# Optimization experiments

Measured on AMD Instinct MI355X. Metric: run time of the kernel, lower is better.

## Reference

```python
import jax, jax.numpy as jnp
import numpy as np


def _grid_neighbors(H, W):
    # 4-neighbor grid adjacency for the Mesh([H, W]) graph
    idx = np.arange(H * W).reshape(H, W)
    p = np.full((H + 2, W + 2), -1, dtype=np.int64)
    p[1:-1, 1:-1] = idx
    nbrs = np.stack([p[0:H, 1:W + 1], p[2:H + 2, 1:W + 1], p[1:H + 1, 0:W], p[1:H + 1, 2:W + 2]], axis=-1).reshape(H * W, 4)
    mask = (nbrs >= 0).astype(np.float32)
    return np.where(nbrs >= 0, nbrs, 0), mask, mask.sum(-1) + 1.0


def _conv(x, w, b):
    y = jax.lax.conv_general_dilated(x, w, (1, 1), 'SAME', dimension_numbers=('NCHW', 'OIHW', 'NCHW'))
    return y + b[None, :, None, None]


def _dconv(x, w1, b1, w2, b2):
    return jax.nn.relu(_conv(jax.nn.relu(_conv(x, w1, b1)), w2, b2))


def _maxpool(x):
    return jax.lax.reduce_window(x, -jnp.inf, jax.lax.max, (1, 1, 2, 2), (1, 1, 2, 2), 'VALID')


def _convT(x, w, b):
    # kernel=2, stride=2 transposed conv (non-overlapping upsample)
    y = jax.lax.conv_transpose(x, w, (2, 2), 'VALID', dimension_numbers=('NCHW', 'HWIO', 'NCHW'))
    return y + b[None, :, None, None]


def _gconv(X, W, b, nbrs, mask, deg):
    # mesh graph conv: D^-1 (A + I) X W, irregular gather over grid adjacency
    g = X[:, nbrs, :]                                          # [B, N, 4, C]
    agg = ((g * mask[None, :, :, None]).sum(2) + X) / deg[None, :, None]
    return jax.nn.relu(jnp.einsum('bnc,cd->bnd', agg, W) + b[None, None, :])


def _forward(x, d1w1, d1b1, d1w2, d1b2, d2w1, d2b1, d2w2, d2b2, md1w, md1b, md2w, md2b, mbw, mbb, mu1w, mu1b, mu2w, mu2b, u3tw, u3tb, u3w1, u3b1, u3w2, u3b2, u4tw, u4tb, u4w1, u4b1, u4w2, u4b2, ow, ob):
    b1 = _dconv(x, d1w1, d1b1, d1w2, d1b2)                     # [1,64,256,256]
    b2 = _dconv(_maxpool(b1), d2w1, d2b1, d2w2, d2b2)          # [1,128,128,128]
    fe = _maxpool(b2)                                           # [1,128,64,64]
    fe = jnp.pad(fe, ((0, 0), (0, 0), (1, 1), (1, 1)))          # pad -> 66x66
    B, C, Hm, Wm = fe.shape
    nbrs, mask, deg = _grid_neighbors(Hm, Wm)
    nbrs, mask, deg = jnp.asarray(nbrs), jnp.asarray(mask), jnp.asarray(deg)
    X = fe.reshape(B, C, Hm * Wm).transpose(0, 2, 1)            # [1, 4356, 128]
    bp1 = _gconv(X, md1w, md1b, nbrs, mask, deg)                # 256 (skip)
    bp2 = _gconv(bp1, md2w, md2b, nbrs, mask, deg)              # 512 (skip)
    Xb = _gconv(bp2, mbw, mbb, nbrs, mask, deg)                 # 1024 mesh bottleneck
    X = _gconv(Xb, mu1w, mu1b, nbrs, mask, deg) + bp2           # 512
    X = _gconv(X, mu2w, mu2b, nbrs, mask, deg) + bp1            # 256
    fe = X.transpose(0, 2, 1).reshape(B, 256, Hm, Wm)[:, :, 1:-1, 1:-1]  # unpad -> 64x64
    u3 = _convT(fe, u3tw, u3tb)                                 # [1,128,128,128]
    fe = _dconv(jnp.concatenate([b2, u3], 1), u3w1, u3b1, u3w2, u3b2)
    u4 = _convT(fe, u4tw, u4tb)                                 # [1,64,256,256]
    fe = _dconv(jnp.concatenate([b1, u4], 1), u4w1, u4b1, u4w2, u4b2)
    return _conv(fe, ow, ob)[:, 0]                              # [1,256,256]


def setup_inputs():
    ks = iter(jax.random.split(jax.random.key(0), 40))
    def W(shape, fan_in):
        return jax.random.normal(next(ks), shape, jnp.float32) * np.float32(np.sqrt(2.0 / fan_in))
    def Z(n):
        return jnp.zeros((n,), jnp.float32)
    return {
        'x': jax.random.normal(next(ks), (1, 3, 256, 256), jnp.float32),
        'd1w1': W((64, 3, 3, 3), 27), 'd1b1': Z(64), 'd1w2': W((64, 64, 3, 3), 576), 'd1b2': Z(64),
        'd2w1': W((128, 64, 3, 3), 576), 'd2b1': Z(128), 'd2w2': W((128, 128, 3, 3), 1152), 'd2b2': Z(128),
        'md1w': W((128, 256), 128), 'md1b': Z(256),
        'md2w': W((256, 512), 256), 'md2b': Z(512),
        'mbw': W((512, 1024), 512), 'mbb': Z(1024),
        'mu1w': W((1024, 512), 1024), 'mu1b': Z(512),
        'mu2w': W((512, 256), 512), 'mu2b': Z(256),
        'u3tw': W((2, 2, 256, 128), 1024), 'u3tb': Z(128),
        'u3w1': W((128, 256, 3, 3), 2304), 'u3b1': Z(128), 'u3w2': W((128, 128, 3, 3), 1152), 'u3b2': Z(128),
        'u4tw': W((2, 2, 128, 64), 512), 'u4tb': Z(64),
        'u4w1': W((64, 128, 3, 3), 1152), 'u4b1': Z(64), 'u4w2': W((64, 64, 3, 3), 576), 'u4b2': Z(64),
        'ow': W((1, 64, 3, 3), 576), 'ob': Z(1),
    }


def reference(x, d1w1, d1b1, d1w2, d1b2, d2w1, d2b1, d2w2, d2b2, md1w, md1b, md2w, md2b, mbw, mbb, mu1w, mu1b, mu2w, mu2b, u3tw, u3tb, u3w1, u3b1, u3w2, u3b2, u4tw, u4tb, u4w1, u4b1, u4w2, u4b2, ow, ob):
    return _forward(x, d1w1, d1b1, d1w2, d1b2, d2w1, d2b1, d2w2, d2b2, md1w, md1b, md2w, md2b, mbw, mbb, mu1w, mu1b, mu2w, mu2b, u3tw, u3tb, u3w1, u3b1, u3w2, u3b2, u4tw, u4tb, u4w1, u4b1, u4w2, u4b2, ow, ob)
```

## Files before the change

### kernel.cpp

```cpp
#include <hip/hip_runtime.h>
#include <cstddef>

#define TPB 256

typedef __attribute__((ext_vector_type(8))) short short8;
typedef __attribute__((ext_vector_type(4))) float f32x4;

__device__ inline unsigned short f2bf(float f) {
    unsigned int u = __builtin_bit_cast(unsigned int, f);
    u += 0x7fffu + ((u >> 16) & 1u);
    return (unsigned short)(u >> 16);
}
__device__ inline float bf2f(unsigned short h) {
    unsigned int u = ((unsigned int)h) << 16;
    return __builtin_bit_cast(float, u);
}

struct TapOffs { int o[9]; };

template<int CHUNKS>
__global__ __launch_bounds__(TPB) void k_conv3f(
    const unsigned short* __restrict__ A0, const unsigned short* __restrict__ Wf,
    const float* __restrict__ bias, unsigned short* __restrict__ O0,
    int AP, int tilesX, int OMS, int OP, int NTtot)
{
    constexpr int Cs  = CHUNKS * 64;
    constexpr int KC2 = CHUNKS * 2;
    __shared__ unsigned short Bs[2][CHUNKS * 4096];

    int lane = threadIdx.x & 63, wave = threadIdx.x >> 6;
    int ml = lane & 15, kq = lane >> 4;
    int nb = blockIdx.y;
    int tileX = blockIdx.x % tilesX, gy = blockIdx.x / tilesX;
    int gx0 = tileX * 64 + wave * 16;

    const unsigned short* Abase = A0 + (size_t)(gy - 1) * AP
                                     + (size_t)(gx0 + ml - 1) * Cs + kq * 8;

    f32x4 acc[4];
    #pragma unroll
    for (int nt = 0; nt < 4; ++nt) acc[nt] = (f32x4){0.f, 0.f, 0.f, 0.f};

    auto stageB = [&](int tap, int buf) {
        unsigned short* bd = Bs[buf];
        #pragma unroll
        for (int it = 0; it < CHUNKS * 2; ++it) {
            int u = threadIdx.x + it * TPB;
            int e = u * 8;
            int ch = e >> 12;
            int rem = e & 4095;
            int q = rem >> 11;
            int rem2 = rem & 2047;
            int ntg = rem2 >> 9;
            int r = rem2 & 511;
            const unsigned short* src = Wf
                + ((size_t)(tap * KC2 + ch * 2 + q) * NTtot + nb * 4 + ntg) * 512 + r;
            *(int4*)&bd[e] = *(const int4*)src;
        }
    };

    stageB(0, 0);
    __syncthreads();
    #pragma unroll
    for (int tap = 0; tap < 9; ++tap) {
        if (tap < 8) stageB(tap + 1, (tap + 1) & 1);
        int ky = tap / 3, kx = tap - (tap / 3) * 3;
        const unsigned short* Ar = Abase + (size_t)ky * AP + kx * Cs;
        const unsigned short* Bb = &Bs[tap & 1][lane * 8];
        #pragma unroll
        for (int ch = 0; ch < CHUNKS; ++ch) {
            #pragma unroll
            for (int q = 0; q < 2; ++q) {
                short8 b[4];
                #pragma unroll
                for (int nt = 0; nt < 4; ++nt)
                    b[nt] = *(const short8*)(Bb + ch * 4096 + q * 2048 + nt * 512);
                short8 a = *(const short8*)(Ar + ch * 64 + q * 32);
                #pragma unroll
                for (int nt = 0; nt < 4; ++nt)
                    acc[nt] = __builtin_amdgcn_mfma_f32_16x16x32_bf16(a, b[nt], acc[nt], 0, 0, 0);
            }
        }
        __syncthreads();
    }

    unsigned short* Orow = O0 + (size_t)gy * OP + (size_t)nb * 64;
    int gx = gx0 + kq * 4;
    #pragma unroll
    for (int nt = 0; nt < 4; ++nt) {
        float bv = bias[nb * 64 + nt * 16 + ml];
        #pragma unroll
        for (int r = 0; r < 4; ++r) {
            float v = fmaxf(acc[nt][r] + bv, 0.f);
            Orow[(size_t)(gx + r) * OMS + nt * 16 + ml] = f2bf(v);
        }
    }
}

template<int KCW>
__global__ __launch_bounds__(TPB) void k_gemmS(
    const unsigned short* __restrict__ A0, const unsigned short* __restrict__ Wf,
    const float* __restrict__ bias, const unsigned short* __restrict__ resid,
    unsigned short* __restrict__ O0, int NTtot,
    int AP, int Wimg, int OMS, int OP, int relu, int ct, int ctDy, int ctDx)
{
    constexpr int K = KCW * 128;
    __shared__ float red[12 * 4 * 64 * 4];
    int lane = threadIdx.x & 63, wave = threadIdx.x >> 6;
    int ml = lane & 15, kq = lane >> 4;
    int m0 = blockIdx.x * 64, nb = blockIdx.y;

    const unsigned short* Wb = Wf;
    unsigned short* Ob = O0;
    if (ct) {
        int tp = blockIdx.z;
        Wb += (size_t)(tp * KCW * 4) * NTtot * 512;
        int dy = 1 - (tp >> 1), dx = 1 - (tp & 1);
        Ob += (size_t)dy * ctDy + (size_t)dx * ctDx;
    }

    const unsigned short* Ap[4];
    #pragma unroll
    for (int i = 0; i < 4; ++i) {
        int mf = (wave + i) & 3;
        int m = m0 + mf * 16;
        int y = m / Wimg, x = m - y * Wimg;
        Ap[i] = A0 + (size_t)y * AP + (size_t)(x + ml) * K + wave * (KCW * 32) + kq * 8;
    }
    const unsigned short* Bp = Wb + ((size_t)(wave * KCW) * NTtot + nb * 4) * 512 + lane * 8;

    f32x4 acc[4][4];
    #pragma unroll
    for (int i = 0; i < 4; ++i)
        #pragma unroll
        for (int nt = 0; nt < 4; ++nt) acc[i][nt] = (f32x4){0.f, 0.f, 0.f, 0.f};

    #pragma unroll
    for (int q = 0; q < KCW; ++q) {
        short8 b[4];
        #pragma unroll
        for (int nt = 0; nt < 4; ++nt)
            b[nt] = *(const short8*)(Bp + ((size_t)q * NTtot + nt) * 512);
        short8 a[4];
        #pragma unroll
        for (int i = 0; i < 4; ++i)
            a[i] = *(const short8*)(Ap[i] + q * 32);
        #pragma unroll
        for (int i = 0; i < 4; ++i)
            #pragma unroll
            for (int nt = 0; nt < 4; ++nt)
                acc[i][nt] = __builtin_amdgcn_mfma_f32_16x16x32_bf16(a[i], b[nt], acc[i][nt], 0, 0, 0);
    }

    #pragma unroll
    for (int i = 1; i < 4; ++i) {
        int s = wave * 3 + (i - 1);
        #pragma unroll
        for (int nt = 0; nt < 4; ++nt)
            *(f32x4*)&red[(((s * 4 + nt) * 64) + lane) * 4] = acc[i][nt];
    }
    __syncthreads();
    #pragma unroll
    for (int w2 = 0; w2 < 4; ++w2) {
        if (w2 == wave) continue;
        int i = (wave - w2) & 3;
        int s = w2 * 3 + (i - 1);
        #pragma unroll
        for (int nt = 0; nt < 4; ++nt) {
            f32x4 v = *(const f32x4*)&red[(((s * 4 + nt) * 64) + lane) * 4];
            acc[0][nt] += v;
        }
    }

    int mrow = m0 + wave * 16 + kq * 4;
    int y = mrow / Wimg, x = mrow - y * Wimg;
    unsigned short* Ot = Ob + (size_t)y * OP + (size_t)x * OMS + nb * 64;
    const unsigned short* Rt = resid ? resid + (size_t)mrow * OMS + nb * 64 : nullptr;
    #pragma unroll
    for (int nt = 0; nt < 4; ++nt) {
        float bv = bias[nb * 64 + nt * 16 + ml];
        #pragma unroll
        for (int r = 0; r < 4; ++r) {
            float v = acc[0][nt][r] + bv;
            if (relu) v = fmaxf(v, 0.f);
            if (Rt) v += bf2f(Rt[(size_t)r * OMS + nt * 16 + ml]);
            Ot[(size_t)r * OMS + nt * 16 + ml] = f2bf(v);
        }
    }
}

template<int KC>
__global__ __launch_bounds__(TPB) void k_gemmN(
    const unsigned short* __restrict__ A0, const unsigned short* __restrict__ Wf,
    const float* __restrict__ bias, unsigned short* __restrict__ O0,
    int Cs, int AP, int Wimg, int OMS, int OP, int NTtot, int relu,
    int ct, int ctDy, int ctDx)
{
    int lane = threadIdx.x & 63, wave = threadIdx.x >> 6;
    int ml = lane & 15, kq = lane >> 4;
    int nb = blockIdx.y;

    const unsigned short* Wb = Wf;
    unsigned short* Ob = O0;
    if (ct) {
        int tp = blockIdx.z;
        Wb += (size_t)(tp * KC) * NTtot * 512;
        int dy = 1 - (tp >> 1), dx = 1 - (tp & 1);
        Ob += (size_t)dy * ctDy + (size_t)dx * ctDx;
    }
    int m0 = blockIdx.x * 64 + wave * 16;
    int y = m0 / Wimg, x = m0 - y * Wimg;
    const unsigned short* Arow = A0 + (size_t)y * AP + (size_t)(x + ml) * Cs + kq * 8;
    const unsigned short* Bp = Wb + (size_t)(nb * 4) * 512 + lane * 8;

    f32x4 acc[4];
    #pragma unroll
    for (int nt = 0; nt < 4; ++nt) acc[nt] = (f32x4){0.f, 0.f, 0.f, 0.f};

    #pragma unroll
    for (int q = 0; q < KC; ++q) {
        short8 b[4];
        #pragma unroll
        for (int nt = 0; nt < 4; ++nt)
            b[nt] = *(const short8*)(Bp + ((size_t)q * NTtot + nt) * 512);
        short8 a = *(const short8*)(Arow + q * 32);
        #pragma unroll
        for (int nt = 0; nt < 4; ++nt)
            acc[nt] = __builtin_amdgcn_mfma_f32_16x16x32_bf16(a, b[nt], acc[nt], 0, 0, 0);
    }

    unsigned short* Ot = Ob + (size_t)y * OP + (size_t)(x + kq * 4) * OMS + (size_t)nb * 64;
    #pragma unroll
    for (int nt = 0; nt < 4; ++nt) {
        float bv = bias[nb * 64 + nt * 16 + ml];
        #pragma unroll
        for (int r = 0; r < 4; ++r) {
            float v = acc[nt][r] + bv;
            if (relu) v = fmaxf(v, 0.f);
            Ot[(size_t)r * OMS + nt * 16 + ml] = f2bf(v);
        }
    }
}

template<int MW, int KC>
__global__ __launch_bounds__(TPB) void k_gemm(
    const unsigned short* __restrict__ A0, const unsigned short* __restrict__ Wf,
    const float* __restrict__ bias, unsigned short* __restrict__ O0,
    int Cs, int AP, int Wimg, int OMS, int OP,
    int T, TapOffs toffs, int NTtot, int relu)
{
    int lane = threadIdx.x & 63, wave = threadIdx.x >> 6;
    int ml = lane & 15, kq = lane >> 4;
    int nb = blockIdx.y;
    const unsigned short* WbB = Wf + (size_t)(nb * 4) * 512 + lane * 8;

    int fy[MW], fx[MW];
    const unsigned short* Af[MW];
    #pragma unroll
    for (int f = 0; f < MW; ++f) {
        int mf = (blockIdx.x * 4 + wave) * (16 * MW) + f * 16;
        int y = mf / Wimg, x = mf - y * Wimg;
        fy[f] = y; fx[f] = x;
        Af[f] = A0 + (size_t)y * AP + (size_t)(x + ml) * Cs + kq * 8;
    }

    f32x4 acc[MW][4];
    #pragma unroll
    for (int f = 0; f < MW; ++f)
        #pragma unroll
        for (int nt = 0; nt < 4; ++nt) acc[f][nt] = (f32x4){0.f, 0.f, 0.f, 0.f};

    for (int tp = 0; tp < T; ++tp) {
        int toff = toffs.o[tp];
        const unsigned short* Wt = WbB + (size_t)(tp * KC) * NTtot * 512;
        #pragma unroll
        for (int q = 0; q < KC; ++q) {
            short8 b[4];
            #pragma unroll
            for (int nt = 0; nt < 4; ++nt)
                b[nt] = *(const short8*)(Wt + (size_t)q * NTtot * 512 + nt * 512);
            short8 a[MW];
            #pragma unroll
            for (int f = 0; f < MW; ++f)
                a[f] = *(const short8*)(Af[f] + toff + q * 32);
            #pragma unroll
            for (int f = 0; f < MW; ++f)
                #pragma unroll
                for (int nt = 0; nt < 4; ++nt)
                    acc[f][nt] = __builtin_amdgcn_mfma_f32_16x16x32_bf16(a[f], b[nt], acc[f][nt], 0, 0, 0);
        }
    }

    #pragma unroll
    for (int f = 0; f < MW; ++f) {
        unsigned short* Ot = O0 + (size_t)fy[f] * OP + (size_t)(fx[f] + kq * 4) * OMS + (size_t)nb * 64;
        #pragma unroll
        for (int nt = 0; nt < 4; ++nt) {
            float bv = bias[nb * 64 + nt * 16 + ml];
            #pragma unroll
            for (int r = 0; r < 4; ++r) {
                float v = acc[f][nt][r] + bv;
                if (relu) v = fmaxf(v, 0.f);
                Ot[(size_t)r * OMS + nt * 16 + ml] = f2bf(v);
            }
        }
    }
}

struct PackArgs {
    const float* w[15];
    int cum[16];
    int mode[15], KC[15], NT[15], K[15], N[15];
};
__global__ __launch_bounds__(TPB) void k_pack_all(
    PackArgs pa, unsigned short* __restrict__ dst, int total)
{
    int idx = blockIdx.x * TPB + threadIdx.x;
    if (idx >= total) return;
    int e = 0;
    #pragma unroll
    for (int i = 1; i < 15; ++i) e += (idx >= pa.cum[i]);
    int local = idx - pa.cum[e];
    const float* w = pa.w[e];
    int KC = pa.KC[e], NT = pa.NT[e], K = pa.K[e], N = pa.N[e], mode = pa.mode[e];

    int j = local & 7, l = (local >> 3) & 63;
    int r = local >> 9;
    int ntg = r % NT; int r2 = r / NT;
    int q = r2 % KC; int tp = r2 / KC;
    int k = q * 32 + (l >> 4) * 8 + j;
    int n = ntg * 16 + (l & 15);
    float v = 0.f;
    if (mode == 0) { int ky = tp / 3, kx = tp % 3; v = w[(size_t)(n * K + k) * 9 + ky * 3 + kx]; }
    else if (mode == 1) { v = w[(size_t)k * N + n]; }
    else if (mode == 2) { v = w[((size_t)tp * K + k) * N + n]; }
    else { if (k < 27) { int tap = k / 3, c = k % 3; int ky = tap / 3, kx = tap % 3;
                         v = w[((n * 3 + c) * 3 + ky) * 3 + kx]; } }
    dst[idx] = f2bf(v);
}

struct ZArgs { int off[10]; int cum[11]; int W2[10]; int H2[10]; int Cs[10]; };
__global__ __launch_bounds__(TPB) void k_zero_all(
    ZArgs za, unsigned short* __restrict__ W, int total)
{
    int idx = blockIdx.x * TPB + threadIdx.x;
    if (idx >= total) return;
    int e = 0;
    #pragma unroll
    for (int i = 1; i < 10; ++i) e += (idx >= za.cum[i]);
    int local = idx - za.cum[e];
    int W2 = za.W2[e], H2 = za.H2[e], Cs = za.Cs[e];
    int topbot = 2 * W2 * Cs;
    int iy, ix, c;
    if (local < topbot) {
        int row = local / (W2 * Cs); int rest = local - row * (W2 * Cs);
        iy = row ? (H2 - 1) : 0; ix = rest / Cs; c = rest - (rest / Cs) * Cs;
    } else {
        int idx2 = local - topbot;
        int per = (H2 - 2) * Cs;
        int side = idx2 / per; int rest = idx2 - side * per;
        iy = 1 + rest / Cs; ix = side ? (W2 - 1) : 0; c = rest - (rest / Cs) * Cs;
    }
    W[(size_t)za.off[e] + ((size_t)iy * W2 + ix) * Cs + c] = 0;
}

__global__ __launch_bounds__(TPB) void k_im2col(
    const float* __restrict__ x, unsigned short* __restrict__ xcol)
{
    int idx = blockIdx.x * TPB + threadIdx.x;
    if (idx >= 65536 * 32) return;
    int k = idx & 31, m = idx >> 5;
    int y = m >> 8, xx = m & 255;
    float v = 0.f;
    if (k < 27) {
        int tap = k / 3, c = k - tap * 3;
        int ty = tap / 3, tx = tap % 3;
        int yy = y + ty - 1, xp = xx + tx - 1;
        if (yy >= 0 && yy < 256 && xp >= 0 && xp < 256)
            v = x[c * 65536 + yy * 256 + xp];
    }
    xcol[idx] = f2bf(v);
}

__global__ __launch_bounds__(TPB) void k_maxpool(
    const unsigned short* __restrict__ inI, unsigned short* __restrict__ outI,
    int Wo, int C4, int CsIn, int inPitch, int CsOut, int outPitch, int total)
{
    int idx = blockIdx.x * TPB + threadIdx.x;
    if (idx >= total) return;
    int c4 = idx % C4; int p = idx / C4;
    int x = p % Wo, y = p / Wo;
    const unsigned short* ip = inI + (size_t)(2 * y) * inPitch + (size_t)(2 * x) * CsIn + c4 * 4;
    ushort4 a = *(const ushort4*)(ip);
    ushort4 b = *(const ushort4*)(ip + CsIn);
    ushort4 c = *(const ushort4*)(ip + inPitch);
    ushort4 d = *(const ushort4*)(ip + inPitch + CsIn);
    ushort4 o;
    o.x = f2bf(fmaxf(fmaxf(bf2f(a.x), bf2f(b.x)), fmaxf(bf2f(c.x), bf2f(d.x))));
    o.y = f2bf(fmaxf(fmaxf(bf2f(a.y), bf2f(b.y)), fmaxf(bf2f(c.y), bf2f(d.y))));
    o.z = f2bf(fmaxf(fmaxf(bf2f(a.z), bf2f(b.z)), fmaxf(bf2f(c.z), bf2f(d.z))));
    o.w = f2bf(fmaxf(fmaxf(bf2f(a.w), bf2f(b.w)), fmaxf(bf2f(c.w), bf2f(d.w))));
    *(ushort4*)(outI + (size_t)y * outPitch + (size_t)x * CsOut + c4 * 4) = o;
}

__global__ __launch_bounds__(TPB) void k_gagg(
    const unsigned short* __restrict__ X, unsigned short* __restrict__ agg,
    int C, int total)
{
    int idx = blockIdx.x * TPB + threadIdx.x;
    if (idx >= total) return;
    int C4 = C >> 2;
    int c4 = idx % C4; int n = idx / C4;
    int i = n / 66, j = n - i * 66;
    size_t base = (size_t)n * C + c4 * 4;
    ushort4 s = *(const ushort4*)(X + base);
    float v0 = bf2f(s.x), v1 = bf2f(s.y), v2 = bf2f(s.z), v3 = bf2f(s.w);
    float cnt = 1.f;
    if (i > 0)  { ushort4 u = *(const ushort4*)(X + base - (size_t)66 * C);
                  v0 += bf2f(u.x); v1 += bf2f(u.y); v2 += bf2f(u.z); v3 += bf2f(u.w); cnt += 1.f; }
    if (i < 65) { ushort4 u = *(const ushort4*)(X + base + (size_t)66 * C);
                  v0 += bf2f(u.x); v1 += bf2f(u.y); v2 += bf2f(u.z); v3 += bf2f(u.w); cnt += 1.f; }
    if (j > 0)  { ushort4 u = *(const ushort4*)(X + base - C);
                  v0 += bf2f(u.x); v1 += bf2f(u.y); v2 += bf2f(u.z); v3 += bf2f(u.w); cnt += 1.f; }
    if (j < 65) { ushort4 u = *(const ushort4*)(X + base + C);
                  v0 += bf2f(u.x); v1 += bf2f(u.y); v2 += bf2f(u.z); v3 += bf2f(u.w); cnt += 1.f; }
    float inv = 1.f / cnt;
    ushort4 o;
    o.x = f2bf(v0 * inv); o.y = f2bf(v1 * inv); o.z = f2bf(v2 * inv); o.w = f2bf(v3 * inv);
    *(ushort4*)(agg + base) = o;
}

__global__ __launch_bounds__(TPB) void k_outconv(
    const unsigned short* __restrict__ vI, const float* __restrict__ ow,
    const float* __restrict__ ob, float* __restrict__ out)
{
    __shared__ float wl[576];
    for (int i = threadIdx.x; i < 576; i += TPB) wl[i] = ow[i];
    __syncthreads();
    int p = blockIdx.x * TPB + threadIdx.x;
    int y = p >> 8, x = p & 255;
    float acc = ob[0];
    #pragma unroll
    for (int ky = 0; ky < 3; ++ky)
        #pragma unroll
        for (int kx = 0; kx < 3; ++kx) {
            const unsigned short* ip = vI + (size_t)((y + ky - 1) * 258 + (x + kx - 1)) * 64;
            int wb = ky * 3 + kx;
            for (int c = 0; c < 64; c += 4) {
                ushort4 uv = *(const ushort4*)(ip + c);
                acc += bf2f(uv.x) * wl[c * 9 + wb] + bf2f(uv.y) * wl[(c + 1) * 9 + wb]
                     + bf2f(uv.z) * wl[(c + 2) * 9 + wb] + bf2f(uv.w) * wl[(c + 3) * 9 + wb];
            }
        }
    out[p] = acc;
}

static inline TapOffs zero_toffs() { TapOffs t = {}; return t; }

extern "C" void kernel_launch(void* const* d_in, const int* in_sizes, int n_in,
                              void* d_out, int out_size, void* d_ws, size_t ws_size,
                              hipStream_t stream) {
    const float* x    = (const float*)d_in[0];
    const float* d1w1 = (const float*)d_in[1];  const float* d1b1 = (const float*)d_in[2];
    const float* d1w2 = (const float*)d_in[3];  const float* d1b2 = (const float*)d_in[4];
    const float* d2w1 = (const float*)d_in[5];  const float* d2b1 = (const float*)d_in[6];
    const float* d2w2 = (const float*)d_in[7];  const float* d2b2 = (const float*)d_in[8];
    const float* md1w = (const float*)d_in[9];  const float* md1b = (const float*)d_in[10];
    const float* md2w = (const float*)d_in[11]; const float* md2b = (const float*)d_in[12];
    const float* mbw  = (const float*)d_in[13]; const float* mbb  = (const float*)d_in[14];
    const float* mu1w = (const float*)d_in[15]; const float* mu1b = (const float*)d_in[16];
    const float* mu2w = (const float*)d_in[17]; const float* mu2b = (const float*)d_in[18];
    const float* u3tw = (const float*)d_in[19]; const float* u3tb = (const float*)d_in[20];
    const float* u3w1 = (const float*)d_in[21]; const float* u3b1 = (const float*)d_in[22];
    const float* u3w2 = (const float*)d_in[23]; const float* u3b2 = (const float*)d_in[24];
    const float* u4tw = (const float*)d_in[25]; const float* u4tb = (const float*)d_in[26];
    const float* u4w1 = (const float*)d_in[27]; const float* u4b1 = (const float*)d_in[28];
    const float* u4w2 = (const float*)d_in[29]; const float* u4b2 = (const float*)d_in[30];
    const float* ow   = (const float*)d_in[31]; const float* ob   = (const float*)d_in[32];
    float* out = (float*)d_out;

    unsigned short* W = (unsigned short*)d_ws;

    const size_t XCOL = 0;
    const size_t A1   = 2097152;
    const size_t CAT4 = 6357248;
    const size_t P1   = 14877440;
    const size_t T2   = 15959040;
    const size_t CAT3 = 18122240;
    const size_t X0   = 22448640;
    const size_t BP1  = 23006208;
    const size_t BP2  = 24185856;
    const size_t XB   = 26545152;
    const size_t XC   = 31263744;
    const size_t XD   = 33623040;
    const size_t V3A  = 34802688;
    const size_t V3B  = 36965888;
    const size_t V4A  = 39129088;
    const size_t V4B  = 43389184;
    const size_t AGG  = 47649280;
    const size_t WP   = 52367872;

    const size_t a1I   = A1 + 259 * 64;
    const size_t cat4I = CAT4 + 259 * 128;
    const size_t p1I   = P1 + 131 * 64;
    const size_t t2I   = T2 + 131 * 128;
    const size_t cat3I = CAT3 + 131 * 256;
    const size_t X0I   = X0 + 67 * 128;
    const size_t XdI   = XD + 67 * 256;
    const size_t v3aI  = V3A + 131 * 128;
    const size_t v3bI  = V3B + 131 * 128;
    const size_t v4aI  = V4A + 259 * 64;
    const size_t v4bI  = V4B + 259 * 64;

    dim3 blk(TPB);
    const int BIG = 1 << 28;

    {
        ZArgs za;
        const int off[10] = {(int)A1,(int)CAT4,(int)P1,(int)T2,(int)CAT3,(int)V3A,(int)V3B,(int)V4A,(int)V4B,(int)X0};
        const int w2 [10] = {258,258,130,130,130,130,130,258,258,66};
        const int h2 [10] = {258,258,130,130,130,130,130,258,258,66};
        const int cs [10] = {64,128,64,128,256,128,128,64,64,128};
        int cum = 0;
        for (int i = 0; i < 10; ++i) {
            za.off[i]=off[i]; za.W2[i]=w2[i]; za.H2[i]=h2[i]; za.Cs[i]=cs[i];
            za.cum[i]=cum; cum += (w2[i]*h2[i] - (w2[i]-2)*(h2[i]-2))*cs[i];
        }
        za.cum[10]=cum;
        k_zero_all<<<dim3((cum + TPB - 1) / TPB), blk, 0, stream>>>(za, W, cum);
    }

    {
        PackArgs pa;
        const float* ws_[15] = {d1w1,d1w2,d2w1,d2w2,md1w,md2w,mbw,mu1w,mu2w,u3tw,u3w1,u3w2,u4tw,u4w1,u4w2};
        const int mode[15] = {3,0,0,0,1,1,1,1,1,2,0,0,2,0,0};
        const int kc [15] = {1,2,2,4,4,8,16,32,16,8,8,4,4,4,2};
        const int nt [15] = {4,4,8,8,16,32,64,32,16,8,8,8,4,4,4};
        const int kk [15] = {32,64,64,128,128,256,512,1024,512,256,256,128,128,128,64};
        const int nn [15] = {64,64,128,128,256,512,1024,512,256,128,128,128,64,64,64};
        const int tt [15] = {1,9,9,9,1,1,1,1,1,4,9,9,4,9,9};
        int cum = 0;
        for (int i = 0; i < 15; ++i) {
            pa.w[i]=ws_[i]; pa.mode[i]=mode[i]; pa.KC[i]=kc[i]; pa.NT[i]=nt[i];
            pa.K[i]=kk[i]; pa.N[i]=nn[i]; pa.cum[i]=cum;
            cum += tt[i]*kc[i]*nt[i]*512;
        }
        pa.cum[15]=cum;
        k_pack_all<<<dim3((cum + TPB - 1) / TPB), blk, 0, stream>>>(pa, W + WP, cum);
    }
    const size_t pw_d1w1=WP+0, pw_d1w2=WP+2048, pw_d2w1=WP+38912, pw_d2w2=WP+112640,
        pw_md1=WP+260096, pw_md2=WP+292864, pw_mb=WP+423936, pw_mu1=WP+948224,
        pw_mu2=WP+1472512, pw_u3t=WP+1603584, pw_u3w1=WP+1734656, pw_u3w2=WP+2029568,
        pw_u4t=WP+2177024, pw_u4w1=WP+2209792, pw_u4w2=WP+2283520;

    k_im2col<<<dim3(8192), blk, 0, stream>>>(x, W + XCOL);
    k_gemm<2,1><<<dim3(512,1), blk, 0, stream>>>(W + XCOL, W + pw_d1w1, d1b1,
        W + a1I, 32, 8192, 256, 64, 258*64, 1, zero_toffs(), 4, 1);
    k_conv3f<1><<<dim3(1024,1), blk, 0, stream>>>(W + a1I, W + pw_d1w2, d1b2,
        W + cat4I, 258*64, 4, 128, 258*128, 4);
    k_maxpool<<<dim3(1024), blk, 0, stream>>>(W + cat4I, W + p1I, 128, 16, 128, 258*128, 64, 130*64, 128*128*16);
    k_conv3f<1><<<dim3(256,2), blk, 0, stream>>>(W + p1I, W + pw_d2w1, d2b1,
        W + t2I, 130*64, 2, 128, 130*128, 8);
    k_conv3f<2><<<dim3(256,2), blk, 0, stream>>>(W + t2I, W + pw_d2w2, d2b2,
        W + cat3I, 130*128, 2, 256, 130*256, 8);
    k_maxpool<<<dim3(512), blk, 0, stream>>>(W + cat3I, W + X0I, 64, 32, 256, 130*256, 128, 66*128, 64*64*32);

    k_gagg<<<dim3(545), blk, 0, stream>>>(W + X0, W + AGG, 128, 4356*32);
    k_gemmS<1><<<dim3(72,4), blk, 0, stream>>>(W + AGG, W + pw_md1, md1b, nullptr,
        W + BP1, 16, 0, BIG, 256, 0, 1, 0, 0, 0);
    k_gagg<<<dim3(1089), blk, 0, stream>>>(W + BP1, W + AGG, 256, 4356*64);
    k_gemmS<2><<<dim3(72,8), blk, 0, stream>>>(W + AGG, W + pw_md2, md2b, nullptr,
        W + BP2, 32, 0, BIG, 512, 0, 1, 0, 0, 0);
    k_gagg<<<dim3(2178), blk, 0, stream>>>(W + BP2, W + AGG, 512, 4356*128);
    k_gemmS<4><<<dim3(72,16), blk, 0, stream>>>(W + AGG, W + pw_mb, mbb, nullptr,
        W + XB, 64, 0, BIG, 1024, 0, 1, 0, 0, 0);
    k_gagg<<<dim3(4356), blk, 0, stream>>>(W + XB, W + AGG, 1024, 4356*256);
    k_gemmS<8><<<dim3(72,8), blk, 0, stream>>>(W + AGG, W + pw_mu1, mu1b, W + BP2,
        W + XC, 32, 0, BIG, 512, 0, 1, 0, 0, 0);
    k_gagg<<<dim3(2178), blk, 0, stream>>>(W + XC, W + AGG, 512, 4356*128);
    k_gemmS<4><<<dim3(72,4), blk, 0, stream>>>(W + AGG, W + pw_mu2, mu2b, W + BP1,
        W + XD, 16, 0, BIG, 256, 0, 1, 0, 0, 0);

    k_gemmS<2><<<dim3(64,2,4), blk, 0, stream>>>(W + XdI, W + pw_u3t, u3tb, nullptr,
        W + cat3I + 128, 8, 66*256, 64, 512, 2*130*256, 0, 1, 130*256, 256);
    k_conv3f<4><<<dim3(256,2), blk, 0, stream>>>(W + cat3I, W + pw_u3w1, u3b1,
        W + v3aI, 130*256, 2, 128, 130*128, 8);
    k_conv3f<2><<<dim3(256,2), blk, 0, stream>>>(W + v3aI, W + pw_u3w2, u3b2,
        W + v3bI, 130*128, 2, 128, 130*128, 8);

    k_gemmN<4><<<dim3(256,1,4), blk, 0, stream>>>(W + v3bI, W + pw_u4t, u4tb,
        W + cat4I + 64, 128, 130*128, 128, 256, 2*258*128, 4, 0, 1, 258*128, 128);
    k_conv3f<2><<<dim3(1024,1), blk, 0, stream>>>(W + cat4I, W + pw_u4w1, u4b1,
        W + v4aI, 258*128, 4, 64, 258*64, 4);
    k_conv3f<1><<<dim3(1024,1), blk, 0, stream>>>(W + v4aI, W + pw_u4w2, u4b2,
        W + v4bI, 258*64, 4, 64, 258*64, 4);

    k_outconv<<<dim3(256), blk, 0, stream>>>(W + v4bI, ow, ob, out);
}
```

Baseline: 396.2 us.

## Fuse mesh graph neighbor aggregation into the graph-conv GEMM A-operand load

Drops the separate k_gagg kernels and the AGG scratch buffer. Each graph-conv GEMM now builds its A operand on the fly: it loads the node and its four grid neighbours, masks out-of-grid ones, sums and scales by the inverse degree, then feeds the MFMA. This removes five launches and a write plus re-read of the aggregated activations. In exchange every N-tile block recomputes the aggregation and issues five times as many A loads, which should mostly hit L2. Masked-out neighbours are still read, before and after the buffer edges, and the zero mask would pass a NaN or Inf found there into the result.

```diff
diff --git a/kernel.cpp b/kernel.cpp
--- a/kernel.cpp
+++ b/kernel.cpp
@@ -97,7 +97,7 @@
     }
 }
 
-template<int KCW>
+template<int KCW, int AGGF>
 __global__ __launch_bounds__(TPB) void k_gemmS(
     const unsigned short* __restrict__ A0, const unsigned short* __restrict__ Wf,
     const float* __restrict__ bias, const unsigned short* __restrict__ resid,
@@ -120,12 +120,24 @@
     }
 
     const unsigned short* Ap[4];
+    float mU[4], mD[4], mL[4], mR[4], inv[4];
     #pragma unroll
     for (int i = 0; i < 4; ++i) {
         int mf = (wave + i) & 3;
         int m = m0 + mf * 16;
-        int y = m / Wimg, x = m - y * Wimg;
-        Ap[i] = A0 + (size_t)y * AP + (size_t)(x + ml) * K + wave * (KCW * 32) + kq * 8;
+        if (AGGF) {
+            int n = m + ml;
+            int ir = n / 66, jc = n - ir * 66;
+            mU[i] = (ir > 0)  ? 1.f : 0.f;
+            mD[i] = (ir < 65) ? 1.f : 0.f;
+            mL[i] = (jc > 0)  ? 1.f : 0.f;
+            mR[i] = (jc < 65) ? 1.f : 0.f;
+            inv[i] = 1.f / (1.f + mU[i] + mD[i] + mL[i] + mR[i]);
+            Ap[i] = A0 + (size_t)n * K + wave * (KCW * 32) + kq * 8;
+        } else {
+            int y = m / Wimg, x = m - y * Wimg;
+            Ap[i] = A0 + (size_t)y * AP + (size_t)(x + ml) * K + wave * (KCW * 32) + kq * 8;
+        }
     }
     const unsigned short* Bp = Wb + ((size_t)(wave * KCW) * NTtot + nb * 4) * 512 + lane * 8;
 
@@ -143,8 +155,29 @@
             b[nt] = *(const short8*)(Bp + ((size_t)q * NTtot + nt) * 512);
         short8 a[4];
         #pragma unroll
-        for (int i = 0; i < 4; ++i)
-            a[i] = *(const short8*)(Ap[i] + q * 32);
+        for (int i = 0; i < 4; ++i) {
+            const unsigned short* p = Ap[i] + q * 32;
+            if (!AGGF) {
+                a[i] = *(const short8*)p;
+            } else {
+                short8 s0 = *(const short8*)p;
+                short8 s1 = *(const short8*)(p - (size_t)66 * K);
+                short8 s2 = *(const short8*)(p + (size_t)66 * K);
+                short8 s3 = *(const short8*)(p - K);
+                short8 s4 = *(const short8*)(p + K);
+                short8 o;
+                #pragma unroll
+                for (int e = 0; e < 8; ++e) {
+                    float v = bf2f((unsigned short)s0[e]);
+                    v = fmaf(mU[i], bf2f((unsigned short)s1[e]), v);
+                    v = fmaf(mD[i], bf2f((unsigned short)s2[e]), v);
+                    v = fmaf(mL[i], bf2f((unsigned short)s3[e]), v);
+                    v = fmaf(mR[i], bf2f((unsigned short)s4[e]), v);
+                    o[e] = (short)f2bf(v * inv[i]);
+                }
+                a[i] = o;
+            }
+        }
         #pragma unroll
         for (int i = 0; i < 4; ++i)
             #pragma unroll
@@ -401,33 +434,6 @@
     o.z = f2bf(fmaxf(fmaxf(bf2f(a.z), bf2f(b.z)), fmaxf(bf2f(c.z), bf2f(d.z))));
     o.w = f2bf(fmaxf(fmaxf(bf2f(a.w), bf2f(b.w)), fmaxf(bf2f(c.w), bf2f(d.w))));
     *(ushort4*)(outI + (size_t)y * outPitch + (size_t)x * CsOut + c4 * 4) = o;
-}
-
-__global__ __launch_bounds__(TPB) void k_gagg(
-    const unsigned short* __restrict__ X, unsigned short* __restrict__ agg,
-    int C, int total)
-{
-    int idx = blockIdx.x * TPB + threadIdx.x;
-    if (idx >= total) return;
-    int C4 = C >> 2;
-    int c4 = idx % C4; int n = idx / C4;
-    int i = n / 66, j = n - i * 66;
-    size_t base = (size_t)n * C + c4 * 4;
-    ushort4 s = *(const ushort4*)(X + base);
-    float v0 = bf2f(s.x), v1 = bf2f(s.y), v2 = bf2f(s.z), v3 = bf2f(s.w);
-    float cnt = 1.f;
-    if (i > 0)  { ushort4 u = *(const ushort4*)(X + base - (size_t)66 * C);
-                  v0 += bf2f(u.x); v1 += bf2f(u.y); v2 += bf2f(u.z); v3 += bf2f(u.w); cnt += 1.f; }
-    if (i < 65) { ushort4 u = *(const ushort4*)(X + base + (size_t)66 * C);
-                  v0 += bf2f(u.x); v1 += bf2f(u.y); v2 += bf2f(u.z); v3 += bf2f(u.w); cnt += 1.f; }
-    if (j > 0)  { ushort4 u = *(const ushort4*)(X + base - C);
-                  v0 += bf2f(u.x); v1 += bf2f(u.y); v2 += bf2f(u.z); v3 += bf2f(u.w); cnt += 1.f; }
-    if (j < 65) { ushort4 u = *(const ushort4*)(X + base + C);
-                  v0 += bf2f(u.x); v1 += bf2f(u.y); v2 += bf2f(u.z); v3 += bf2f(u.w); cnt += 1.f; }
-    float inv = 1.f / cnt;
-    ushort4 o;
-    o.x = f2bf(v0 * inv); o.y = f2bf(v1 * inv); o.z = f2bf(v2 * inv); o.w = f2bf(v3 * inv);
-    *(ushort4*)(agg + base) = o;
 }
 
 __global__ __launch_bounds__(TPB) void k_outconv(
@@ -497,7 +503,6 @@
     const size_t V3B  = 36965888;
     const size_t V4A  = 39129088;
     const size_t V4B  = 43389184;
-    const size_t AGG  = 47649280;
     const size_t WP   = 52367872;
 
     const size_t a1I   = A1 + 259 * 64;
@@ -565,23 +570,18 @@
         W + cat3I, 130*128, 2, 256, 130*256, 8);
     k_maxpool<<<dim3(512), blk, 0, stream>>>(W + cat3I, W + X0I, 64, 32, 256, 130*256, 128, 66*128, 64*64*32);
 
-    k_gagg<<<dim3(545), blk, 0, stream>>>(W + X0, W + AGG, 128, 4356*32);
-    k_gemmS<1><<<dim3(72,4), blk, 0, stream>>>(W + AGG, W + pw_md1, md1b, nullptr,
+    k_gemmS<1,1><<<dim3(72,4), blk, 0, stream>>>(W + X0, W + pw_md1, md1b, nullptr,
         W + BP1, 16, 0, BIG, 256, 0, 1, 0, 0, 0);
-    k_gagg<<<dim3(1089), blk, 0, stream>>>(W + BP1, W + AGG, 256, 4356*64);
-    k_gemmS<2><<<dim3(72,8), blk, 0, stream>>>(W + AGG, W + pw_md2, md2b, nullptr,
+    k_gemmS<2,1><<<dim3(72,8), blk, 0, stream>>>(W + BP1, W + pw_md2, md2b, nullptr,
         W + BP2, 32, 0, BIG, 512, 0, 1, 0, 0, 0);
-    k_gagg<<<dim3(2178), blk, 0, stream>>>(W + BP2, W + AGG, 512, 4356*128);
-    k_gemmS<4><<<dim3(72,16), blk, 0, stream>>>(W + AGG, W + pw_mb, mbb, nullptr,
+    k_gemmS<4,1><<<dim3(72,16), blk, 0, stream>>>(W + BP2, W + pw_mb, mbb, nullptr,
         W + XB, 64, 0, BIG, 1024, 0, 1, 0, 0, 0);
-    k_gagg<<<dim3(4356), blk, 0, stream>>>(W + XB, W + AGG, 1024, 4356*256);
-    k_gemmS<8><<<dim3(72,8), blk, 0, stream>>>(W + AGG, W + pw_mu1, mu1b, W + BP2,
+    k_gemmS<8,1><<<dim3(72,8), blk, 0, stream>>>(W + XB, W + pw_mu1, mu1b, W + BP2,
         W + XC, 32, 0, BIG, 512, 0, 1, 0, 0, 0);
-    k_gagg<<<dim3(2178), blk, 0, stream>>>(W + XC, W + AGG, 512, 4356*128);
-    k_gemmS<4><<<dim3(72,4), blk, 0, stream>>>(W + AGG, W + pw_mu2, mu2b, W + BP1,
+    k_gemmS<4,1><<<dim3(72,4), blk, 0, stream>>>(W + XC, W + pw_mu2, mu2b, W + BP1,
         W + XD, 16, 0, BIG, 256, 0, 1, 0, 0, 0);
 
-    k_gemmS<2><<<dim3(64,2,4), blk, 0, stream>>>(W + XdI, W + pw_u3t, u3tb, nullptr,
+    k_gemmS<2,0><<<dim3(64,2,4), blk, 0, stream>>>(W + XdI, W + pw_u3t, u3tb, nullptr,
         W + cat3I + 128, 8, 66*256, 64, 512, 2*130*256, 0, 1, 130*256, 256);
     k_conv3f<4><<<dim3(256,2), blk, 0, stream>>>(W + cat3I, W + pw_u3w1, u3b1,
         W + v3aI, 130*256, 2, 128, 130*128, 8);
```

Measured after the change: 468.9 us. 18.3% more time.

## Switch 3x3 conv kernels to 32x32x16 MFMA with 2x2 wave tiling

Applied to the files above, without the earlier changes.

Replaces the 16x16x32 bf16 MFMA conv kernel, where each wave computed 16 pixels x 64 channels, with a 32x32x16 variant where waves form a 2x2 grid of 32 pixels x 32 channels. The weight pack kernel gains a new layout mode for the 32-wide fragments, and all 3x3 conv launches are switched to it. The aim is fewer LDS B-fragment reads per MFMA and more output per instruction, in exchange for the larger 32x32 MFMA and a different A/B reuse pattern.

```diff
diff --git a/kernel.cpp b/kernel.cpp
--- a/kernel.cpp
+++ b/kernel.cpp
@@ -5,6 +5,7 @@
 
 typedef __attribute__((ext_vector_type(8))) short short8;
 typedef __attribute__((ext_vector_type(4))) float f32x4;
+typedef __attribute__((ext_vector_type(16))) float f32x16;
 
 __device__ inline unsigned short f2bf(float f) {
     unsigned int u = __builtin_bit_cast(unsigned int, f);
@@ -19,27 +20,28 @@
 struct TapOffs { int o[9]; };
 
 template<int CHUNKS>
-__global__ __launch_bounds__(TPB) void k_conv3f(
+__global__ __launch_bounds__(TPB) void k_conv32(
     const unsigned short* __restrict__ A0, const unsigned short* __restrict__ Wf,
     const float* __restrict__ bias, unsigned short* __restrict__ O0,
-    int AP, int tilesX, int OMS, int OP, int NTtot)
-{
-    constexpr int Cs  = CHUNKS * 64;
-    constexpr int KC2 = CHUNKS * 2;
+    int AP, int tilesX, int OMS, int OP, int NT32)
+{
+    constexpr int Cs   = CHUNKS * 64;
+    constexpr int KC16 = CHUNKS * 4;
     __shared__ unsigned short Bs[2][CHUNKS * 4096];
 
     int lane = threadIdx.x & 63, wave = threadIdx.x >> 6;
-    int ml = lane & 15, kq = lane >> 4;
+    int ml = lane & 31, kh = lane >> 5;
+    int mi = wave >> 1, ni = wave & 1;
     int nb = blockIdx.y;
     int tileX = blockIdx.x % tilesX, gy = blockIdx.x / tilesX;
-    int gx0 = tileX * 64 + wave * 16;
+    int gx0 = tileX * 64 + mi * 32;
 
     const unsigned short* Abase = A0 + (size_t)(gy - 1) * AP
-                                     + (size_t)(gx0 + ml - 1) * Cs + kq * 8;
-
-    f32x4 acc[4];
-    #pragma unroll
-    for (int nt = 0; nt < 4; ++nt) acc[nt] = (f32x4){0.f, 0.f, 0.f, 0.f};
+                                     + (size_t)(gx0 + ml - 1) * Cs + kh * 8;
+
+    f32x16 acc;
+    #pragma unroll
+    for (int i = 0; i < 16; ++i) acc[i] = 0.f;
 
     auto stageB = [&](int tap, int buf) {
         unsigned short* bd = Bs[buf];
@@ -49,12 +51,12 @@
             int e = u * 8;
             int ch = e >> 12;
             int rem = e & 4095;
-            int q = rem >> 11;
-            int rem2 = rem & 2047;
-            int ntg = rem2 >> 9;
+            int s = rem >> 10;
+            int rem2 = rem & 1023;
+            int nt = rem2 >> 9;
             int r = rem2 & 511;
             const unsigned short* src = Wf
-                + ((size_t)(tap * KC2 + ch * 2 + q) * NTtot + nb * 4 + ntg) * 512 + r;
+                + ((size_t)(tap * KC16 + ch * 4 + s) * NT32 + nb * 2 + nt) * 512 + r;
             *(int4*)&bd[e] = *(const int4*)src;
         }
     };
@@ -66,34 +68,27 @@
         if (tap < 8) stageB(tap + 1, (tap + 1) & 1);
         int ky = tap / 3, kx = tap - (tap / 3) * 3;
         const unsigned short* Ar = Abase + (size_t)ky * AP + kx * Cs;
-        const unsigned short* Bb = &Bs[tap & 1][lane * 8];
+        const unsigned short* Bb = &Bs[tap & 1][ni * 512 + lane * 8];
         #pragma unroll
         for (int ch = 0; ch < CHUNKS; ++ch) {
             #pragma unroll
-            for (int q = 0; q < 2; ++q) {
-                short8 b[4];
-                #pragma unroll
-                for (int nt = 0; nt < 4; ++nt)
-                    b[nt] = *(const short8*)(Bb + ch * 4096 + q * 2048 + nt * 512);
-                short8 a = *(const short8*)(Ar + ch * 64 + q * 32);
-                #pragma unroll
-                for (int nt = 0; nt < 4; ++nt)
-                    acc[nt] = __builtin_amdgcn_mfma_f32_16x16x32_bf16(a, b[nt], acc[nt], 0, 0, 0);
+            for (int s = 0; s < 4; ++s) {
+                short8 b = *(const short8*)(Bb + (ch * 4 + s) * 1024);
+                short8 a = *(const short8*)(Ar + ch * 64 + s * 16);
+                acc = __builtin_amdgcn_mfma_f32_32x32x16_bf16(a, b, acc, 0, 0, 0);
             }
         }
         __syncthreads();
     }
 
-    unsigned short* Orow = O0 + (size_t)gy * OP + (size_t)nb * 64;
-    int gx = gx0 + kq * 4;
-    #pragma unroll
-    for (int nt = 0; nt < 4; ++nt) {
-        float bv = bias[nb * 64 + nt * 16 + ml];
-        #pragma unroll
-        for (int r = 0; r < 4; ++r) {
-            float v = fmaxf(acc[nt][r] + bv, 0.f);
-            Orow[(size_t)(gx + r) * OMS + nt * 16 + ml] = f2bf(v);
-        }
+    int nbase = nb * 64 + ni * 32;
+    unsigned short* Orow = O0 + (size_t)gy * OP + nbase + ml;
+    float bv = bias[nbase + ml];
+    #pragma unroll
+    for (int r = 0; r < 16; ++r) {
+        int row = (r & 3) + 8 * (r >> 2) + 4 * kh;
+        float v = fmaxf(acc[r] + bv, 0.f);
+        Orow[(size_t)(gx0 + row) * OMS] = f2bf(v);
     }
 }
 
@@ -328,14 +323,21 @@
     int r = local >> 9;
     int ntg = r % NT; int r2 = r / NT;
     int q = r2 % KC; int tp = r2 / KC;
-    int k = q * 32 + (l >> 4) * 8 + j;
-    int n = ntg * 16 + (l & 15);
     float v = 0.f;
-    if (mode == 0) { int ky = tp / 3, kx = tp % 3; v = w[(size_t)(n * K + k) * 9 + ky * 3 + kx]; }
-    else if (mode == 1) { v = w[(size_t)k * N + n]; }
-    else if (mode == 2) { v = w[((size_t)tp * K + k) * N + n]; }
-    else { if (k < 27) { int tap = k / 3, c = k % 3; int ky = tap / 3, kx = tap % 3;
-                         v = w[((n * 3 + c) * 3 + ky) * 3 + kx]; } }
+    if (mode == 4) {
+        int k = q * 16 + (l >> 5) * 8 + j;
+        int n = ntg * 32 + (l & 31);
+        int ky = tp / 3, kx = tp % 3;
+        v = w[(size_t)(n * K + k) * 9 + ky * 3 + kx];
+    } else {
+        int k = q * 32 + (l >> 4) * 8 + j;
+        int n = ntg * 16 + (l & 15);
+        if (mode == 0) { int ky = tp / 3, kx = tp % 3; v = w[(size_t)(n * K + k) * 9 + ky * 3 + kx]; }
+        else if (mode == 1) { v = w[(size_t)k * N + n]; }
+        else if (mode == 2) { v = w[((size_t)tp * K + k) * N + n]; }
+        else { if (k < 27) { int tap = k / 3, c = k % 3; int ky = tap / 3, kx = tap % 3;
+                             v = w[((n * 3 + c) * 3 + ky) * 3 + kx]; } }
+    }
     dst[idx] = f2bf(v);
 }
 
@@ -533,9 +535,9 @@
     {
         PackArgs pa;
         const float* ws_[15] = {d1w1,d1w2,d2w1,d2w2,md1w,md2w,mbw,mu1w,mu2w,u3tw,u3w1,u3w2,u4tw,u4w1,u4w2};
-        const int mode[15] = {3,0,0,0,1,1,1,1,1,2,0,0,2,0,0};
-        const int kc [15] = {1,2,2,4,4,8,16,32,16,8,8,4,4,4,2};
-        const int nt [15] = {4,4,8,8,16,32,64,32,16,8,8,8,4,4,4};
+        const int mode[15] = {3,4,4,4,1,1,1,1,1,2,4,4,2,4,4};
+        const int kc [15] = {1,4,4,8,4,8,16,32,16,8,16,8,4,8,4};
+        const int nt [15] = {4,2,4,4,16,32,64,32,16,8,4,4,4,2,2};
         const int kk [15] = {32,64,64,128,128,256,512,1024,512,256,256,128,128,128,64};
         const int nn [15] = {64,64,128,128,256,512,1024,512,256,128,128,128,64,64,64};
         const int tt [15] = {1,9,9,9,1,1,1,1,1,4,9,9,4,9,9};
@@ -556,13 +558,13 @@
     k_im2col<<<dim3(8192), blk, 0, stream>>>(x, W + XCOL);
     k_gemm<2,1><<<dim3(512,1), blk, 0, stream>>>(W + XCOL, W + pw_d1w1, d1b1,
         W + a1I, 32, 8192, 256, 64, 258*64, 1, zero_toffs(), 4, 1);
-    k_conv3f<1><<<dim3(1024,1), blk, 0, stream>>>(W + a1I, W + pw_d1w2, d1b2,
-        W + cat4I, 258*64, 4, 128, 258*128, 4);
+    k_conv32<1><<<dim3(1024,1), blk, 0, stream>>>(W + a1I, W + pw_d1w2, d1b2,
+        W + cat4I, 258*64, 4, 128, 258*128, 2);
     k_maxpool<<<dim3(1024), blk, 0, stream>>>(W + cat4I, W + p1I, 128, 16, 128, 258*128, 64, 130*64, 128*128*16);
-    k_conv3f<1><<<dim3(256,2), blk, 0, stream>>>(W + p1I, W + pw_d2w1, d2b1,
-        W + t2I, 130*64, 2, 128, 130*128, 8);
-    k_conv3f<2><<<dim3(256,2), blk, 0, stream>>>(W + t2I, W + pw_d2w2, d2b2,
-        W + cat3I, 130*128, 2, 256, 130*256, 8);
+    k_conv32<1><<<dim3(256,2), blk, 0, stream>>>(W + p1I, W + pw_d2w1, d2b1,
+        W + t2I, 130*64, 2, 128, 130*128, 4);
+    k_conv32<2><<<dim3(256,2), blk, 0, stream>>>(W + t2I, W + pw_d2w2, d2b2,
+        W + cat3I, 130*128, 2, 256, 130*256, 4);
     k_maxpool<<<dim3(512), blk, 0, stream>>>(W + cat3I, W + X0I, 64, 32, 256, 130*256, 128, 66*128, 64*64*32);
 
     k_gagg<<<dim3(545), blk, 0, stream>>>(W + X0, W + AGG, 128, 4356*32);
@@ -583,17 +585,17 @@
 
     k_gemmS<2><<<dim3(64,2,4), blk, 0, stream>>>(W + XdI, W + pw_u3t, u3tb, nullptr,
         W + cat3I + 128, 8, 66*256, 64, 512, 2*130*256, 0, 1, 130*256, 256);
-    k_conv3f<4><<<dim3(256,2), blk, 0, stream>>>(W + cat3I, W + pw_u3w1, u3b1,
-        W + v3aI, 130*256, 2, 128, 130*128, 8);
-    k_conv3f<2><<<dim3(256,2), blk, 0, stream>>>(W + v3aI, W + pw_u3w2, u3b2,
-        W + v3bI, 130*128, 2, 128, 130*128, 8);
+    k_conv32<4><<<dim3(256,2), blk, 0, stream>>>(W + cat3I, W + pw_u3w1, u3b1,
+        W + v3aI, 130*256, 2, 128, 130*128, 4);
+    k_conv32<2><<<dim3(256,2), blk, 0, stream>>>(W + v3aI, W + pw_u3w2, u3b2,
+        W + v3bI, 130*128, 2, 128, 130*128, 4);
 
     k_gemmN<4><<<dim3(256,1,4), blk, 0, stream>>>(W + v3bI, W + pw_u4t, u4tb,
         W + cat4I + 64, 128, 130*128, 128, 256, 2*258*128, 4, 0, 1, 258*128, 128);
-    k_conv3f<2><<<dim3(1024,1), blk, 0, stream>>>(W + cat4I, W + pw_u4w1, u4b1,
-        W + v4aI, 258*128, 4, 64, 258*64, 4);
-    k_conv3f<1><<<dim3(1024,1), blk, 0, stream>>>(W + v4aI, W + pw_u4w2, u4b2,
-        W + v4bI, 258*64, 4, 64, 258*64, 4);
+    k_conv32<2><<<dim3(1024,1), blk, 0, stream>>>(W + cat4I, W + pw_u4w1, u4b1,
+        W + v4aI, 258*128, 4, 64, 258*64, 2);
+    k_conv32<1><<<dim3(1024,1), blk, 0, stream>>>(W + v4aI, W + pw_u4w2, u4b2,
+        W + v4bI, 258*64, 4, 64, 258*64, 2);
 
     k_outconv<<<dim3(256), blk, 0, stream>>>(W + v4bI, ow, ob, out);
 }
```

New measurement: 451.9 us. 14.0% more time.
